# Kernel optimization log

Measured on AMD Instinct MI355X. Metric: run time of the kernel, lower is better.

## Reference

```python
import jax, jax.numpy as jnp
import numpy as np

B, N, F, H, E = 2, 20000, 128, 1, 640000
C = F  # out_channels per head (concat=False -> mean over heads)
NEG_SLOPE = 0.2


def setup_inputs() -> dict:
    key = jax.random.key(0)
    k = jax.random.split(key, 6)
    x = jax.random.normal(k[0], (B, N, F), dtype=jnp.float32)
    edge_index = jax.random.randint(k[1], (2, E), 0, N, dtype=jnp.int64)
    s = 1.0 / np.sqrt(F)
    W = jax.random.normal(k[2], (H * C, F), dtype=jnp.float32) * s      # PyG Linear weight
    att_src = jax.random.normal(k[3], (H, C), dtype=jnp.float32) * s
    att_dst = jax.random.normal(k[4], (H, C), dtype=jnp.float32) * s
    bias = jnp.zeros((C,), dtype=jnp.float32)
    return {"x": x, "edge_index": edge_index, "W": W,
            "att_src": att_src, "att_dst": att_dst, "bias": bias}


def _gat_single(x, src, dst, W, att_src, att_dst, bias):
    # x: [N, F]; src/dst: [E'] (self-loops already appended)
    h = (x @ W.T).reshape(N, H, C)                      # [N, H, C]
    a_src = jnp.einsum('nhc,hc->nh', h, att_src)        # [N, H]
    a_dst = jnp.einsum('nhc,hc->nh', h, att_dst)        # [N, H]
    logits = jax.nn.leaky_relu(a_src[src] + a_dst[dst], NEG_SLOPE)  # [E', H]
    # edge-softmax over incoming edges of each dst node
    seg_max = jax.ops.segment_max(logits, dst, num_segments=N)      # [N, H]
    e = jnp.exp(logits - seg_max[dst])
    denom = jax.ops.segment_sum(e, dst, num_segments=N)             # [N, H]
    alpha = e / denom[dst]                                          # [E', H]
    msg = h[src] * alpha[:, :, None]                                # [E', H, C]
    out = jax.ops.segment_sum(msg, dst, num_segments=N)             # [N, H, C]
    return out.mean(axis=1) + bias                                  # [N, C]


def reference(x, edge_index, W, att_src, att_dst, bias):
    # PyG GATConv default: add self-loops
    loops = jnp.arange(N, dtype=edge_index.dtype)
    src = jnp.concatenate([edge_index[0], loops])
    dst = jnp.concatenate([edge_index[1], loops])
    f = lambda xb: _gat_single(xb, src, dst, W, att_src, att_dst, bias)
    return jax.vmap(f)(x)  # [B, N, F]
```

## Files before the change

### kernel.cpp

```cpp
#include <hip/hip_runtime.h>
#include <hip/hip_bf16.h>
#include <math.h>

#define BB    2
#define NN    20000
#define FF    128
#define EE    640000
#define EP    (EE + NN)
#define CAP   128
#define SLOPE 0.2f

typedef __attribute__((ext_vector_type(8))) short bf16x8;
typedef __attribute__((ext_vector_type(4))) float f32x4;

static __device__ __forceinline__ ushort f2bf(float f) {
    unsigned u = __float_as_uint(f);
    u += 0x7fffu + ((u >> 16) & 1u);
    return (ushort)(u >> 16);
}
static __device__ __forceinline__ float bf2f(unsigned hw) {
    return __uint_as_float(hw << 16);
}
static __device__ __forceinline__ float bflo(unsigned q) {
    return __uint_as_float(q << 16);
}
static __device__ __forceinline__ float bfhi(unsigned q) {
    return __uint_as_float(q & 0xffff0000u);
}

__global__ __launch_bounds__(256) void gemm_att_kernel(
    const float* __restrict__ x, const float* __restrict__ W,
    const float* __restrict__ att_src, const float* __restrict__ att_dst,
    unsigned* __restrict__ hbu, float* __restrict__ as2, float* __restrict__ ad2,
    int* __restrict__ cnt)
{
    __shared__ ushort XL[64 * 128];
    __shared__ ushort WL[128 * 128];
    const int tid = threadIdx.x;
    const int r0 = blockIdx.x * 64;

    if (blockIdx.x < 79) {
        int i = blockIdx.x * 256 + tid;
        if (i < NN) cnt[i] = 0;
    }

    {
        const float4* xg = (const float4*)(x + (size_t)r0 * 128);
        #pragma unroll
        for (int i = 0; i < 8; ++i) {
            int idx = tid + i * 256;
            int r = idx >> 5, k = (idx & 31) * 4;
            float4 v = xg[idx];
            ushort4 p = { f2bf(v.x), f2bf(v.y), f2bf(v.z), f2bf(v.w) };
            unsigned byte = ((unsigned)r << 8) + ((unsigned)k << 1);
            byte ^= (unsigned)(r & 7) << 4;
            *(ushort4*)((char*)XL + byte) = p;
        }
    }
    {
        const float4* wg = (const float4*)W;
        #pragma unroll
        for (int i = 0; i < 16; ++i) {
            int idx = tid + i * 256;
            int c = idx >> 5, k = (idx & 31) * 4;
            float4 v = wg[idx];
            ushort4 p = { f2bf(v.x), f2bf(v.y), f2bf(v.z), f2bf(v.w) };
            unsigned byte = ((unsigned)c << 8) + ((unsigned)k << 1);
            byte ^= (unsigned)(c & 7) << 4;
            *(ushort4*)((char*)WL + byte) = p;
        }
    }
    __syncthreads();

    const int wid = tid >> 6, lane = tid & 63;
    const int l15 = lane & 15, lg = lane >> 4;
    f32x4 acc[8];
    #pragma unroll
    for (int i = 0; i < 8; ++i) acc[i] = (f32x4){0.f, 0.f, 0.f, 0.f};

    const int arow = wid * 16 + l15;
    #pragma unroll
    for (int kt = 0; kt < 4; ++kt) {
        unsigned abyte = ((unsigned)arow << 8) + (unsigned)(kt * 64 + lg * 16);
        abyte ^= (unsigned)(arow & 7) << 4;
        bf16x8 af = *(const bf16x8*)((const char*)XL + abyte);
        #pragma unroll
        for (int ct = 0; ct < 8; ++ct) {
            int c = ct * 16 + l15;
            unsigned bbyte = ((unsigned)c << 8) + (unsigned)(kt * 64 + lg * 16);
            bbyte ^= (unsigned)(c & 7) << 4;
            bf16x8 bfr = *(const bf16x8*)((const char*)WL + bbyte);
            acc[ct] = __builtin_amdgcn_mfma_f32_16x16x32_bf16(af, bfr, acc[ct], 0, 0, 0);
        }
    }

    float ps0=0,ps1=0,ps2=0,ps3=0, pd0=0,pd1=0,pd2=0,pd3=0;
    #pragma unroll
    for (int ct = 0; ct < 8; ++ct) {
        int c = ct * 16 + l15;
        float as_ = att_src[c], ad_ = att_dst[c];
        ps0 += acc[ct][0]*as_; pd0 += acc[ct][0]*ad_;
        ps1 += acc[ct][1]*as_; pd1 += acc[ct][1]*ad_;
        ps2 += acc[ct][2]*as_; pd2 += acc[ct][2]*ad_;
        ps3 += acc[ct][3]*as_; pd3 += acc[ct][3]*ad_;
    }
    #pragma unroll
    for (int o = 1; o < 16; o <<= 1) {
        ps0 += __shfl_xor(ps0, o, 64); pd0 += __shfl_xor(pd0, o, 64);
        ps1 += __shfl_xor(ps1, o, 64); pd1 += __shfl_xor(pd1, o, 64);
        ps2 += __shfl_xor(ps2, o, 64); pd2 += __shfl_xor(pd2, o, 64);
        ps3 += __shfl_xor(ps3, o, 64); pd3 += __shfl_xor(pd3, o, 64);
    }
    if (l15 == 0) {
        int rb = r0 + wid * 16 + lg * 4;
        #pragma unroll
        for (int q = 0; q < 4; ++q) {
            int r = rb + q;
            int b = (r >= NN);
            int n = r - b * NN;
            float ps = q==0?ps0 : q==1?ps1 : q==2?ps2 : ps3;
            float pd = q==0?pd0 : q==1?pd1 : q==2?pd2 : pd3;
            as2[n * 2 + b] = ps;
            ad2[n * 2 + b] = pd;
        }
    }

    __syncthreads();
    ushort* hl = (ushort*)WL;
    {
        int rb = wid * 16 + lg * 4;
        #pragma unroll
        for (int ct = 0; ct < 8; ++ct) {
            int c = ct * 16 + l15;
            hl[(rb+0) * 128 + c] = f2bf(acc[ct][0]);
            hl[(rb+1) * 128 + c] = f2bf(acc[ct][1]);
            hl[(rb+2) * 128 + c] = f2bf(acc[ct][2]);
            hl[(rb+3) * 128 + c] = f2bf(acc[ct][3]);
        }
    }
    __syncthreads();
    {
        const unsigned* hs = (const unsigned*)hl;
        #pragma unroll
        for (int i = 0; i < 16; ++i) {
            int idx = tid + i * 256;
            int row = idx >> 6, p = idx & 63;
            int r = r0 + row;
            int b = (r >= NN);
            int n = r - b * NN;
            hbu[(size_t)n * 128 + p * 2 + b] = hs[row * 64 + p];
        }
    }
}

__global__ __launch_bounds__(256) void scatter_kernel(
    const int* __restrict__ ei,
    const float2* __restrict__ as2, const float2* __restrict__ ad2,
    int* __restrict__ cnt, uint2* __restrict__ buck)
{
    int e = blockIdx.x * blockDim.x + threadIdx.x;
    if (e >= EP) return;
    int s, d;
    if (e < EE) {
        s = ei[e]; d = ei[EE + e];
        if ((unsigned)s >= NN || (unsigned)d >= NN) return;
    } else {
        s = d = e - EE;
    }
    float2 av = as2[s];
    float2 dv = ad2[d];
    float l0 = av.x + dv.x; l0 = l0 > 0.f ? l0 : SLOPE * l0;
    float l1 = av.y + dv.y; l1 = l1 > 0.f ? l1 : SLOPE * l1;
    unsigned w0 = f2bf(__expf(l0));
    unsigned w1 = f2bf(__expf(l1));
    int slot = atomicAdd(&cnt[d], 1);
    if (slot < CAP) {
        uint2 rec = { (unsigned)s | (w0 << 16), w1 };
        buck[(size_t)d * CAP + slot] = rec;
    }
}

__global__ __launch_bounds__(256) void gather_kernel(
    const uint2* __restrict__ h,
    const int* __restrict__ cnt, const uint2* __restrict__ buck,
    const float* __restrict__ bias, float* __restrict__ out)
{
    const int tid = threadIdx.x;
    const int wid = tid >> 6, lane = tid & 63;
    const int n = blockIdx.x * 4 + wid;

    __shared__ int    ssrc[4][128];
    __shared__ float2 swp[4][128];

    const int cn = min(cnt[n], CAP);

    float den0 = 0.f, den1 = 0.f;
    #pragma unroll
    for (int r = 0; r < 2; ++r) {
        int j = r * 64 + lane;
        if (j < cn) {
            uint2 rec = buck[(size_t)n * CAP + j];
            float w0 = bf2f(rec.x >> 16);
            float w1 = bf2f(rec.y & 0xffffu);
            ssrc[wid][j] = (int)(rec.x & 0xffffu);
            swp[wid][j] = (float2){w0, w1};
            den0 += w0; den1 += w1;
        }
    }
    #pragma unroll
    for (int o = 32; o > 0; o >>= 1) {
        den0 += __shfl_xor(den0, o, 64);
        den1 += __shfl_xor(den1, o, 64);
    }

    float a0x = 0.f, a0y = 0.f, a1x = 0.f, a1y = 0.f;
    int j = 0;
    for (; j + 3 < cn; j += 4) {
        int s0 = ssrc[wid][j],     s1 = ssrc[wid][j + 1];
        int s2 = ssrc[wid][j + 2], s3 = ssrc[wid][j + 3];
        uint2 q0 = h[(size_t)s0 * 64 + lane];
        uint2 q1 = h[(size_t)s1 * 64 + lane];
        uint2 q2 = h[(size_t)s2 * 64 + lane];
        uint2 q3 = h[(size_t)s3 * 64 + lane];
        float2 w0 = swp[wid][j],     w1 = swp[wid][j + 1];
        float2 w2 = swp[wid][j + 2], w3 = swp[wid][j + 3];
        a0x += w0.x * bflo(q0.x); a0y += w0.x * bfhi(q0.x);
        a1x += w0.y * bflo(q0.y); a1y += w0.y * bfhi(q0.y);
        a0x += w1.x * bflo(q1.x); a0y += w1.x * bfhi(q1.x);
        a1x += w1.y * bflo(q1.y); a1y += w1.y * bfhi(q1.y);
        a0x += w2.x * bflo(q2.x); a0y += w2.x * bfhi(q2.x);
        a1x += w2.y * bflo(q2.y); a1y += w2.y * bfhi(q2.y);
        a0x += w3.x * bflo(q3.x); a0y += w3.x * bfhi(q3.x);
        a1x += w3.y * bflo(q3.y); a1y += w3.y * bfhi(q3.y);
    }
    for (; j < cn; ++j) {
        int s0 = ssrc[wid][j];
        uint2 q0 = h[(size_t)s0 * 64 + lane];
        float2 w0 = swp[wid][j];
        a0x += w0.x * bflo(q0.x); a0y += w0.x * bfhi(q0.x);
        a1x += w0.y * bflo(q0.y); a1y += w0.y * bfhi(q0.y);
    }

    float r0 = 1.f / den0, r1 = 1.f / den1;
    float2 bv = *(const float2*)&bias[lane * 2];
    float2 o0 = { a0x * r0 + bv.x, a0y * r0 + bv.y };
    float2 o1 = { a1x * r1 + bv.x, a1y * r1 + bv.y };
    *(float2*)&out[(size_t)n * 128 + lane * 2]        = o0;
    *(float2*)&out[((size_t)NN + n) * 128 + lane * 2] = o1;
}

extern "C" void kernel_launch(void* const* d_in, const int* in_sizes, int n_in,
                              void* d_out, int out_size, void* d_ws, size_t ws_size,
                              hipStream_t stream)
{
    const float* x       = (const float*)d_in[0];
    const int*   ei      = (const int*)d_in[1];
    const float* W       = (const float*)d_in[2];
    const float* att_src = (const float*)d_in[3];
    const float* att_dst = (const float*)d_in[4];
    const float* bias    = (const float*)d_in[5];
    float* out = (float*)d_out;

    char* ws = (char*)d_ws;
    unsigned* hbu  = (unsigned*)(ws);
    float*    as2  = (float*)(ws + 10240000);
    float*    ad2  = (float*)(ws + 10400000);
    int*      cnt  = (int*)(ws + 10560000);
    uint2*    buck = (uint2*)(ws + 10640000);

    gemm_att_kernel<<<(BB * NN) / 64, 256, 0, stream>>>(x, W, att_src, att_dst,
                                                        hbu, as2, ad2, cnt);
    scatter_kernel<<<(EP + 255) / 256, 256, 0, stream>>>(
        ei, (const float2*)as2, (const float2*)ad2, cnt, buck);
    gather_kernel<<<NN / 4, 256, 0, stream>>>((const uint2*)hbu, cnt, buck,
                                              bias, out);
}
```

Measured before the change: 92.38 us.

## Split edge buckets into four sub-counters and move attention exp into gather

The scatter kernel now stores only a 16-bit source index per edge into one of four per-destination sub-buckets chosen by edge index, which spreads atomic contention across four counters. The leaky-relu/exp weight computation moves from scatter to gather, where as2 is looked up per source. Records shrink from 8 to 2 bytes, scatter threads handle four edges each, and nontemporal loads and stores are used for streaming data. The trade-off is extra gather-side as2 lookups and more counter reads, plus a changed overflow cap of 64 per sub-bucket and 128 total per node.

```diff
diff --git a/kernel.cpp b/kernel.cpp
--- a/kernel.cpp
+++ b/kernel.cpp
@@ -7,20 +7,18 @@
 #define FF    128
 #define EE    640000
 #define EP    (EE + NN)
-#define CAP   128
+#define CAPR  64
 #define SLOPE 0.2f
 
 typedef __attribute__((ext_vector_type(8))) short bf16x8;
 typedef __attribute__((ext_vector_type(4))) float f32x4;
+typedef __attribute__((ext_vector_type(2))) float f32x2;
 
 static __device__ __forceinline__ ushort f2bf(float f) {
     unsigned u = __float_as_uint(f);
     u += 0x7fffu + ((u >> 16) & 1u);
     return (ushort)(u >> 16);
 }
-static __device__ __forceinline__ float bf2f(unsigned hw) {
-    return __uint_as_float(hw << 16);
-}
 static __device__ __forceinline__ float bflo(unsigned q) {
     return __uint_as_float(q << 16);
 }
@@ -32,16 +30,16 @@
     const float* __restrict__ x, const float* __restrict__ W,
     const float* __restrict__ att_src, const float* __restrict__ att_dst,
     unsigned* __restrict__ hbu, float* __restrict__ as2, float* __restrict__ ad2,
-    int* __restrict__ cnt)
+    int* __restrict__ cnt4)
 {
     __shared__ ushort XL[64 * 128];
     __shared__ ushort WL[128 * 128];
     const int tid = threadIdx.x;
     const int r0 = blockIdx.x * 64;
 
-    if (blockIdx.x < 79) {
+    if (blockIdx.x < 313) {
         int i = blockIdx.x * 256 + tid;
-        if (i < NN) cnt[i] = 0;
+        if (i < 4 * NN) cnt4[i] = 0;
     }
 
     {
@@ -154,57 +152,69 @@
 }
 
 __global__ __launch_bounds__(256) void scatter_kernel(
-    const int* __restrict__ ei,
-    const float2* __restrict__ as2, const float2* __restrict__ ad2,
-    int* __restrict__ cnt, uint2* __restrict__ buck)
-{
-    int e = blockIdx.x * blockDim.x + threadIdx.x;
-    if (e >= EP) return;
-    int s, d;
-    if (e < EE) {
-        s = ei[e]; d = ei[EE + e];
-        if ((unsigned)s >= NN || (unsigned)d >= NN) return;
-    } else {
-        s = d = e - EE;
-    }
-    float2 av = as2[s];
-    float2 dv = ad2[d];
-    float l0 = av.x + dv.x; l0 = l0 > 0.f ? l0 : SLOPE * l0;
-    float l1 = av.y + dv.y; l1 = l1 > 0.f ? l1 : SLOPE * l1;
-    unsigned w0 = f2bf(__expf(l0));
-    unsigned w1 = f2bf(__expf(l1));
-    int slot = atomicAdd(&cnt[d], 1);
-    if (slot < CAP) {
-        uint2 rec = { (unsigned)s | (w0 << 16), w1 };
-        buck[(size_t)d * CAP + slot] = rec;
+    const int* __restrict__ ei, int* __restrict__ cnt4, ushort* __restrict__ buck)
+{
+    const int base = blockIdx.x * 1024 + threadIdx.x;
+    #pragma unroll
+    for (int k = 0; k < 4; ++k) {
+        int e = base + k * 256;
+        if (e >= EP) continue;
+        int s, d;
+        if (e < EE) {
+            s = __builtin_nontemporal_load(ei + e);
+            d = __builtin_nontemporal_load(ei + EE + e);
+            if ((unsigned)s >= NN || (unsigned)d >= NN) continue;
+        } else {
+            s = d = e - EE;
+        }
+        int r = e & 3;
+        int slot = atomicAdd(&cnt4[r * NN + d], 1);
+        if (slot < CAPR) {
+            ushort v = (ushort)s;
+            __builtin_nontemporal_store(v, &buck[(((size_t)r * NN + d) << 6) + slot]);
+        }
     }
 }
 
 __global__ __launch_bounds__(256) void gather_kernel(
     const uint2* __restrict__ h,
-    const int* __restrict__ cnt, const uint2* __restrict__ buck,
+    const int* __restrict__ cnt4, const ushort* __restrict__ buck,
+    const float2* __restrict__ as2, const float2* __restrict__ ad2,
     const float* __restrict__ bias, float* __restrict__ out)
 {
     const int tid = threadIdx.x;
     const int wid = tid >> 6, lane = tid & 63;
     const int n = blockIdx.x * 4 + wid;
 
-    __shared__ int    ssrc[4][128];
+    __shared__ ushort ssrc[4][128];
     __shared__ float2 swp[4][128];
 
-    const int cn = min(cnt[n], CAP);
+    const float2 adv = ad2[n];
+    int c0 = min(cnt4[0 * NN + n], CAPR);
+    int c1 = min(cnt4[1 * NN + n], CAPR);
+    int c2 = min(cnt4[2 * NN + n], CAPR);
+    int c3 = min(cnt4[3 * NN + n], CAPR);
+    const int b1 = c0, b2 = c0 + c1, b3 = c0 + c1 + c2;
+    const int cn = min(b3 + c3, 128);
 
     float den0 = 0.f, den1 = 0.f;
     #pragma unroll
-    for (int r = 0; r < 2; ++r) {
-        int j = r * 64 + lane;
-        if (j < cn) {
-            uint2 rec = buck[(size_t)n * CAP + j];
-            float w0 = bf2f(rec.x >> 16);
-            float w1 = bf2f(rec.y & 0xffffu);
-            ssrc[wid][j] = (int)(rec.x & 0xffffu);
-            swp[wid][j] = (float2){w0, w1};
-            den0 += w0; den1 += w1;
+    for (int r = 0; r < 4; ++r) {
+        int cr = r==0?c0 : r==1?c1 : r==2?c2 : c3;
+        int br = r==0?0  : r==1?b1 : r==2?b2 : b3;
+        if (lane < cr) {
+            int idx = br + lane;
+            ushort s = __builtin_nontemporal_load(
+                &buck[(((size_t)r * NN + n) << 6) + lane]);
+            float2 asv = as2[s];
+            float l0 = asv.x + adv.x; l0 = l0 > 0.f ? l0 : SLOPE * l0;
+            float l1 = asv.y + adv.y; l1 = l1 > 0.f ? l1 : SLOPE * l1;
+            float w0 = __expf(l0), w1 = __expf(l1);
+            if (idx < 128) {
+                ssrc[wid][idx] = s;
+                swp[wid][idx] = (float2){w0, w1};
+                den0 += w0; den1 += w1;
+            }
         }
     }
     #pragma unroll
@@ -243,10 +253,12 @@
 
     float r0 = 1.f / den0, r1 = 1.f / den1;
     float2 bv = *(const float2*)&bias[lane * 2];
-    float2 o0 = { a0x * r0 + bv.x, a0y * r0 + bv.y };
-    float2 o1 = { a1x * r1 + bv.x, a1y * r1 + bv.y };
-    *(float2*)&out[(size_t)n * 128 + lane * 2]        = o0;
-    *(float2*)&out[((size_t)NN + n) * 128 + lane * 2] = o1;
+    f32x2 o0 = { a0x * r0 + bv.x, a0y * r0 + bv.y };
+    f32x2 o1 = { a1x * r1 + bv.x, a1y * r1 + bv.y };
+    f32x2* op0 = (f32x2*)&out[(size_t)n * 128 + lane * 2];
+    f32x2* op1 = (f32x2*)&out[((size_t)NN + n) * 128 + lane * 2];
+    __builtin_nontemporal_store(o0, op0);
+    __builtin_nontemporal_store(o1, op1);
 }
 
 extern "C" void kernel_launch(void* const* d_in, const int* in_sizes, int n_in,
@@ -265,13 +277,13 @@
     unsigned* hbu  = (unsigned*)(ws);
     float*    as2  = (float*)(ws + 10240000);
     float*    ad2  = (float*)(ws + 10400000);
-    int*      cnt  = (int*)(ws + 10560000);
-    uint2*    buck = (uint2*)(ws + 10640000);
+    int*      cnt4 = (int*)(ws + 10560000);
+    ushort*   buck = (ushort*)(ws + 10880000);
 
     gemm_att_kernel<<<(BB * NN) / 64, 256, 0, stream>>>(x, W, att_src, att_dst,
-                                                        hbu, as2, ad2, cnt);
-    scatter_kernel<<<(EP + 255) / 256, 256, 0, stream>>>(
-        ei, (const float2*)as2, (const float2*)ad2, cnt, buck);
-    gather_kernel<<<NN / 4, 256, 0, stream>>>((const uint2*)hbu, cnt, buck,
-                                              bias, out);
-}
+                                                        hbu, as2, ad2, cnt4);
+    scatter_kernel<<<(EP + 1023) / 1024, 256, 0, stream>>>(ei, cnt4, buck);
+    gather_kernel<<<NN / 4, 256, 0, stream>>>((const uint2*)hbu, cnt4, buck,
+                                              (const float2*)as2,
+                                              (const float2*)ad2, bias, out);
+}
```

After: 109.4 us. 18.4% more time.

## Replace per-node atomic bucket scatter with two-level bin and in-block counting sort

Applied to the files above, without the earlier changes.

The per-edge global atomic scatter into fixed 128-slot per-node buckets is replaced by a two-pass CSR build. A bin kernel groups edges into 79 coarse bins of 256 destinations, staging them in shared memory so each block does one global atomic per bin. A 79-block sort kernel then counts and places edges per destination in shared memory while computing the attention weights, and writes a compact record array with per-node start and count. This removes heavy global atomic contention and the scattered writes into a sparse bucket array, and packs gather reads contiguously. The cost is an extra memset and kernel launch, only 79 blocks of parallelism in the sort stage, and a fixed BINCAP per bin that may overflow on skewed inputs.

```diff
diff --git a/kernel.cpp b/kernel.cpp
--- a/kernel.cpp
+++ b/kernel.cpp
@@ -7,7 +7,8 @@
 #define FF    128
 #define EE    640000
 #define EP    (EE + NN)
-#define CAP   128
+#define NBIN  79
+#define BINCAP 10240
 #define SLOPE 0.2f
 
 typedef __attribute__((ext_vector_type(8))) short bf16x8;
@@ -31,18 +32,12 @@
 __global__ __launch_bounds__(256) void gemm_att_kernel(
     const float* __restrict__ x, const float* __restrict__ W,
     const float* __restrict__ att_src, const float* __restrict__ att_dst,
-    unsigned* __restrict__ hbu, float* __restrict__ as2, float* __restrict__ ad2,
-    int* __restrict__ cnt)
+    unsigned* __restrict__ hbu, float* __restrict__ as2, float* __restrict__ ad2)
 {
     __shared__ ushort XL[64 * 128];
     __shared__ ushort WL[128 * 128];
     const int tid = threadIdx.x;
     const int r0 = blockIdx.x * 64;
-
-    if (blockIdx.x < 79) {
-        int i = blockIdx.x * 256 + tid;
-        if (i < NN) cnt[i] = 0;
-    }
 
     {
         const float4* xg = (const float4*)(x + (size_t)r0 * 128);
@@ -153,56 +148,140 @@
     }
 }
 
-__global__ __launch_bounds__(256) void scatter_kernel(
-    const int* __restrict__ ei,
+__global__ __launch_bounds__(256) void bin_kernel(
+    const int* __restrict__ ei, int* __restrict__ binCur,
+    unsigned* __restrict__ binbuf)
+{
+    __shared__ int hcnt[NBIN];
+    __shared__ int hofs[NBIN + 1];
+    __shared__ int hbase[NBIN];
+    __shared__ int hcur[NBIN];
+    __shared__ unsigned stage[1024];
+    const int tid = threadIdx.x;
+    for (int i = tid; i < NBIN; i += 256) hcnt[i] = 0;
+    __syncthreads();
+
+    const int e0 = blockIdx.x * 1024;
+    int bin[4]; unsigned word[4];
+    #pragma unroll
+    for (int k = 0; k < 4; ++k) {
+        int e = e0 + k * 256 + tid;
+        bin[k] = -1;
+        if (e < EP) {
+            int s, d; bool ok;
+            if (e < EE) {
+                s = ei[e]; d = ei[EE + e];
+                ok = ((unsigned)s < NN) && ((unsigned)d < NN);
+            } else { s = d = e - EE; ok = true; }
+            if (ok) {
+                bin[k] = d >> 8;
+                word[k] = ((unsigned)(d & 255) << 15) | (unsigned)s;
+                atomicAdd(&hcnt[bin[k]], 1);
+            }
+        }
+    }
+    __syncthreads();
+    if (tid == 0) {
+        int run = 0;
+        for (int b = 0; b < NBIN; ++b) { hofs[b] = run; run += hcnt[b]; }
+        hofs[NBIN] = run;
+    }
+    __syncthreads();
+    if (tid < NBIN) {
+        hbase[tid] = atomicAdd(&binCur[tid], hcnt[tid]);
+        hcur[tid] = 0;
+    }
+    __syncthreads();
+    #pragma unroll
+    for (int k = 0; k < 4; ++k) {
+        if (bin[k] >= 0) {
+            int slot = atomicAdd(&hcur[bin[k]], 1);
+            stage[hofs[bin[k]] + slot] = word[k];
+        }
+    }
+    __syncthreads();
+    const int total = hofs[NBIN];
+    for (int i = tid; i < total; i += 256) {
+        int lo = 0, hi = NBIN;
+        while (hi - lo > 1) { int mid = (lo + hi) >> 1; if (hofs[mid] <= i) lo = mid; else hi = mid; }
+        binbuf[(size_t)lo * BINCAP + hbase[lo] + (i - hofs[lo])] = stage[i];
+    }
+}
+
+__global__ __launch_bounds__(1024) void sort_kernel(
+    const unsigned* __restrict__ binbuf, const int* __restrict__ binCur,
     const float2* __restrict__ as2, const float2* __restrict__ ad2,
-    int* __restrict__ cnt, uint2* __restrict__ buck)
-{
-    int e = blockIdx.x * blockDim.x + threadIdx.x;
-    if (e >= EP) return;
-    int s, d;
-    if (e < EE) {
-        s = ei[e]; d = ei[EE + e];
-        if ((unsigned)s >= NN || (unsigned)d >= NN) return;
-    } else {
-        s = d = e - EE;
-    }
-    float2 av = as2[s];
-    float2 dv = ad2[d];
-    float l0 = av.x + dv.x; l0 = l0 > 0.f ? l0 : SLOPE * l0;
-    float l1 = av.y + dv.y; l1 = l1 > 0.f ? l1 : SLOPE * l1;
-    unsigned w0 = f2bf(__expf(l0));
-    unsigned w1 = f2bf(__expf(l1));
-    int slot = atomicAdd(&cnt[d], 1);
-    if (slot < CAP) {
-        uint2 rec = { (unsigned)s | (w0 << 16), w1 };
-        buck[(size_t)d * CAP + slot] = rec;
+    uint2* __restrict__ rec, int* __restrict__ nodeStart,
+    int* __restrict__ nodeCnt)
+{
+    __shared__ int ncnt[256];
+    __shared__ int nofs[256];
+    __shared__ int ncur[256];
+    const int b = blockIdx.x;
+    const int tid = threadIdx.x;
+    const int cnt = min(binCur[b], BINCAP);
+    const unsigned* src = binbuf + (size_t)b * BINCAP;
+
+    if (tid < 256) ncnt[tid] = 0;
+    __syncthreads();
+    for (int i = tid; i < cnt; i += 1024)
+        atomicAdd(&ncnt[src[i] >> 15], 1);
+    __syncthreads();
+    if (tid == 0) {
+        int run = 0;
+        for (int i = 0; i < 256; ++i) { nofs[i] = run; run += ncnt[i]; }
+    }
+    __syncthreads();
+    if (tid < 256) {
+        int n = b * 256 + tid;
+        if (n < NN) {
+            nodeStart[n] = b * BINCAP + nofs[tid];
+            nodeCnt[n]   = ncnt[tid];
+        }
+        ncur[tid] = 0;
+    }
+    __syncthreads();
+    for (int i = tid; i < cnt; i += 1024) {
+        unsigned w = src[i];
+        int dl = w >> 15;
+        int s  = w & 0x7fff;
+        int d  = b * 256 + dl;
+        float2 av = as2[s];
+        float2 dv = ad2[d];
+        float l0 = av.x + dv.x; l0 = l0 > 0.f ? l0 : SLOPE * l0;
+        float l1 = av.y + dv.y; l1 = l1 > 0.f ? l1 : SLOPE * l1;
+        int slot = atomicAdd(&ncur[dl], 1);
+        uint2 r = { (unsigned)s | ((unsigned)f2bf(__expf(l0)) << 16),
+                    (unsigned)f2bf(__expf(l1)) };
+        rec[(size_t)b * BINCAP + nofs[dl] + slot] = r;
     }
 }
 
 __global__ __launch_bounds__(256) void gather_kernel(
     const uint2* __restrict__ h,
-    const int* __restrict__ cnt, const uint2* __restrict__ buck,
+    const int* __restrict__ nodeStart, const int* __restrict__ nodeCnt,
+    const uint2* __restrict__ rec,
     const float* __restrict__ bias, float* __restrict__ out)
 {
     const int tid = threadIdx.x;
     const int wid = tid >> 6, lane = tid & 63;
     const int n = blockIdx.x * 4 + wid;
 
-    __shared__ int    ssrc[4][128];
+    __shared__ ushort ssrc[4][128];
     __shared__ float2 swp[4][128];
 
-    const int cn = min(cnt[n], CAP);
+    const int beg = nodeStart[n];
+    const int cn = min(nodeCnt[n], 128);
 
     float den0 = 0.f, den1 = 0.f;
     #pragma unroll
     for (int r = 0; r < 2; ++r) {
         int j = r * 64 + lane;
         if (j < cn) {
-            uint2 rec = buck[(size_t)n * CAP + j];
-            float w0 = bf2f(rec.x >> 16);
-            float w1 = bf2f(rec.y & 0xffffu);
-            ssrc[wid][j] = (int)(rec.x & 0xffffu);
+            uint2 rc = rec[(size_t)beg + j];
+            float w0 = bf2f(rc.x >> 16);
+            float w1 = bf2f(rc.y & 0xffffu);
+            ssrc[wid][j] = (ushort)(rc.x & 0xffffu);
             swp[wid][j] = (float2){w0, w1};
             den0 += w0; den1 += w1;
         }
@@ -262,16 +341,22 @@
     float* out = (float*)d_out;
 
     char* ws = (char*)d_ws;
-    unsigned* hbu  = (unsigned*)(ws);
-    float*    as2  = (float*)(ws + 10240000);
-    float*    ad2  = (float*)(ws + 10400000);
-    int*      cnt  = (int*)(ws + 10560000);
-    uint2*    buck = (uint2*)(ws + 10640000);
-
+    unsigned* hbu      = (unsigned*)(ws);
+    float*    as2      = (float*)(ws + 10240000);
+    float*    ad2      = (float*)(ws + 10400000);
+    int*      binCur   = (int*)(ws + 10560000);
+    unsigned* binbuf   = (unsigned*)(ws + 10560512);
+    uint2*    rec      = (uint2*)(ws + 13796352);
+    int*      nodeStart= (int*)(ws + 20268032);
+    int*      nodeCnt  = (int*)(ws + 20348032);
+
+    hipMemsetAsync(binCur, 0, NBIN * sizeof(int), stream);
+    bin_kernel<<<(EP + 1023) / 1024, 256, 0, stream>>>(ei, binCur, binbuf);
     gemm_att_kernel<<<(BB * NN) / 64, 256, 0, stream>>>(x, W, att_src, att_dst,
-                                                        hbu, as2, ad2, cnt);
-    scatter_kernel<<<(EP + 255) / 256, 256, 0, stream>>>(
-        ei, (const float2*)as2, (const float2*)ad2, cnt, buck);
-    gather_kernel<<<NN / 4, 256, 0, stream>>>((const uint2*)hbu, cnt, buck,
-                                              bias, out);
-}
+                                                        hbu, as2, ad2);
+    sort_kernel<<<NBIN, 1024, 0, stream>>>(binbuf, binCur,
+                                           (const float2*)as2, (const float2*)ad2,
+                                           rec, nodeStart, nodeCnt);
+    gather_kernel<<<NN / 4, 256, 0, stream>>>((const uint2*)hbu, nodeStart,
+                                              nodeCnt, rec, bias, out);
+}
```

New measurement: 98.27 us. +6.4%, slower.
